# Performance work log

Measured on AMD Instinct MI355X. Metric: run time of the kernel, lower is better.

Reference implementation:

```python
import jax, jax.numpy as jnp
import numpy as np

EMBED = 1024
HEADS = 16
HEAD_DIM = EMBED // HEADS


def setup_inputs() -> dict:
    key = jax.random.key(0)
    ks = jax.random.split(key, 6)
    N, S = 4, 1024
    query = jax.random.normal(ks[0], (N, S, EMBED), dtype=jnp.float32)
    keys = jax.random.normal(ks[1], (N, S, EMBED), dtype=jnp.float32)
    values = jax.random.normal(ks[2], (N, S, EMBED), dtype=jnp.float32)
    mask = jax.random.randint(ks[3], (N, 1, S, S), 0, 2, dtype=jnp.int32)
    W_out = jax.random.normal(ks[4], (EMBED, EMBED), dtype=jnp.float32) * (1.0 / np.sqrt(EMBED))
    b_out = jax.random.normal(ks[5], (EMBED,), dtype=jnp.float32) * 0.02
    return {"query": query, "keys": keys, "values": values, "mask": mask,
            "W_out": W_out, "b_out": b_out}


def reference(query, keys, values, mask, W_out, b_out):
    N, Q, _ = query.shape
    K = keys.shape[1]
    # NOTE: the torch module never applies its per-head q/k/v Linear layers;
    # only the reshape + attention + fc_out are in the forward path.
    q = query.reshape(N, Q, HEADS, HEAD_DIM)
    k = keys.reshape(N, K, HEADS, HEAD_DIM)
    v = values.reshape(N, K, HEADS, HEAD_DIM)
    # energy: [N, H, Q, K]
    energy = jnp.einsum("bqhd,bkhd->bhqk", q, k)
    energy = jnp.where(mask == 0, jnp.float32(-1e20), energy)
    attn = jax.nn.softmax(energy / jnp.sqrt(jnp.float32(HEAD_DIM)), axis=3)
    out = jnp.einsum("bhqk,bkhd->bqhd", attn, v).reshape(N, Q, HEADS * HEAD_DIM)
    return out @ W_out.T + b_out
```

## Files before the change

### kernel.cpp

```cpp
#include <hip/hip_runtime.h>
#include <math.h>

#define NB 4
#define SL 1024
#define EMB 1024
#define NH 16
#define HD 64
#define QB 128

typedef __attribute__((ext_vector_type(8))) short bf16x8;
typedef __attribute__((ext_vector_type(4))) float f32x4;

static __device__ __forceinline__ unsigned pk2(float a, float b) {
    unsigned x = __float_as_uint(a) + 0x8000u;
    unsigned y = __float_as_uint(b) + 0x8000u;
    return (x >> 16) | (y & 0xFFFF0000u);
}
static __device__ __forceinline__ float exp2_fast(float x) {
    float r; asm("v_exp_f32 %0, %1" : "=v"(r) : "v"(x)); return r;
}
static __device__ __forceinline__ void gload_lds16(const void* g, void* l) {
    __builtin_amdgcn_global_load_lds(
        (const __attribute__((address_space(1))) unsigned int*)g,
        (__attribute__((address_space(3))) unsigned int*)l, 16, 0, 0);
}

__global__ __launch_bounds__(256) void prep(
    const float* __restrict__ W, unsigned short* __restrict__ Wb,
    const float* __restrict__ Kf, unsigned short* __restrict__ Kb,
    const float* __restrict__ V, unsigned short* __restrict__ Vt,
    const int* __restrict__ mask, unsigned long long* __restrict__ Mbt)
{
    __shared__ unsigned short sT[128 * 68];
    const int bid = blockIdx.x, tid = threadIdx.x;

    if (bid < 512) {
        int i = (bid * 256 + tid) * 8;
        float4 f0 = *(const float4*)&W[i];
        float4 f1 = *(const float4*)&W[i + 4];
        uint4 u = { pk2(f0.x,f0.y), pk2(f0.z,f0.w), pk2(f1.x,f1.y), pk2(f1.z,f1.w) };
        *(uint4*)&Wb[i] = u;
    } else if (bid < 2560) {
        int t = bid - 512;
        int b = t >> 9, h = (t >> 5) & 15, k0 = (t & 31) * 32;
        int r = tid >> 3, d = (tid & 7) * 8;
        const float* gp = &Kf[((size_t)(b * SL + k0 + r)) * EMB + h * HD + d];
        float4 f0 = *(const float4*)gp, f1 = *(const float4*)(gp + 4);
        uint4 u = { pk2(f0.x,f0.y), pk2(f0.z,f0.w), pk2(f1.x,f1.y), pk2(f1.z,f1.w) };
        *(uint4*)&Kb[((size_t)((b * NH + h) * SL + k0 + r)) * HD + d] = u;
    } else if (bid < 3072) {
        int t = bid - 2560;
        int bh = t >> 3, kb = t & 7;
        int b = bh >> 4, h = bh & 15;
        int k0 = kb * 128;
        #pragma unroll
        for (int i = 0; i < 4; ++i) {
            int lin = (i * 256 + tid) * 8;
            int r = lin >> 6, d = lin & 63;
            const float* gp = &V[((size_t)(b * SL + k0 + r)) * EMB + h * HD + d];
            float4 f0 = *(const float4*)gp, f1 = *(const float4*)(gp + 4);
            uint2 u0 = { pk2(f0.x,f0.y), pk2(f0.z,f0.w) };
            uint2 u1 = { pk2(f1.x,f1.y), pk2(f1.z,f1.w) };
            *(uint2*)&sT[r * 68 + d]     = u0;
            *(uint2*)&sT[r * 68 + d + 4] = u1;
        }
        __syncthreads();
        #pragma unroll
        for (int p = 0; p < 4; ++p) {
            int d = p * 16 + (tid >> 4);
            int c = tid & 15;
            unsigned v[4];
            #pragma unroll
            for (int j = 0; j < 4; ++j) {
                unsigned lo = sT[(c * 8 + 2 * j) * 68 + d];
                unsigned hi = sT[(c * 8 + 2 * j + 1) * 68 + d];
                v[j] = lo | (hi << 16);
            }
            uint4 u = { v[0], v[1], v[2], v[3] };
            *(uint4*)&Vt[((size_t)(bh * HD + d)) * SL + k0 + c * 8] = u;
        }
    } else {
        int t = bid - 3072;
        int lane = tid & 63;
        #pragma unroll
        for (int r = 0; r < 4; ++r) {
            int wid = (t * 4 + (tid >> 6)) * 4 + r;
            int c = wid & 15, q = (wid >> 4) & 1023, bb = wid >> 14;
            int mv = mask[((size_t)bb * SL + q) * SL + c * 64 + lane];
            unsigned long long bits = __ballot(mv != 0);
            if (lane == 0) Mbt[((size_t)bb * 16 + c) * SL + q] = bits;
        }
    }
}

__global__ __launch_bounds__(256, 2) void attn_mfma(
    const float* __restrict__ Q, const unsigned short* __restrict__ Kb,
    const unsigned short* __restrict__ Vt,
    const unsigned long long* __restrict__ Mbt,
    unsigned short* __restrict__ Oa)
{
    const int q0 = blockIdx.x * QB;
    const int h = blockIdx.y, b = blockIdx.z;
    const int tid = threadIdx.x;
    const int w = tid >> 6, lane = tid & 63;
    const int m16 = lane & 15, quad = lane >> 4;
    const int lr = lane >> 3, lc = lane & 7;
    const int sr0 = tid >> 3;

    __shared__ __align__(16) unsigned short sQ[QB * 64];
    __shared__ __align__(16) unsigned short sK[2][64 * 64];
    __shared__ __align__(16) unsigned short sVt[2][64 * 64];
    __shared__ __align__(16) unsigned short sP[QB * 72];
    __shared__ uint2 lut[16];

    if (tid < 16) {
        unsigned w0 = ((tid & 1) ? 0xFFFFu : 0u) | ((tid & 2) ? 0xFFFF0000u : 0u);
        unsigned w1 = ((tid & 4) ? 0xFFFFu : 0u) | ((tid & 8) ? 0xFFFF0000u : 0u);
        lut[tid] = make_uint2(w0, w1);
    }

    const size_t vbase = (size_t)((b * NH + h) * HD) * SL;
    const size_t kbase = (size_t)((b * NH + h) * SL) * HD;

    #pragma unroll
    for (int i = 0; i < 2; ++i) {
        int row = w * 16 + i * 8;
        gload_lds16(&Vt[vbase + (size_t)(row + lr) * SL + (lc ^ lr) * 8], &sVt[0][row * 64]);
        gload_lds16(&Kb[kbase + (size_t)(row + lr) * HD + (lc ^ lr) * 8], &sK[0][row * 64]);
    }
    #pragma unroll
    for (int it = 0; it < 4; ++it) {
        int r = sr0 + it * 32;
        const float* gp = &Q[((size_t)(b * SL + q0 + r)) * EMB + h * HD + lc * 8];
        float4 f0 = *(const float4*)gp, f1 = *(const float4*)(gp + 4);
        uint4 u = { pk2(f0.x,f0.y), pk2(f0.z,f0.w), pk2(f1.x,f1.y), pk2(f1.z,f1.w) };
        *(uint4*)&sQ[r * 64 + ((lc ^ (r & 7)) * 8)] = u;
    }
    __syncthreads();

    bf16x8 bQ[2][2];
    #pragma unroll
    for (int u = 0; u < 2; ++u) {
        int qrow = w * 32 + u * 16 + m16;
        #pragma unroll
        for (int hh = 0; hh < 2; ++hh)
            bQ[u][hh] = *(const bf16x8*)&sQ[qrow * 64 + (((hh * 4 + quad) ^ (qrow & 7)) * 8)];
    }

    f32x4 O[2][4] = {};
    f32x4 lacc[2] = {};
    const float CSC = 0.125f * 1.44269504f;
    const short one_bf = (short)0x3F80;
    const bf16x8 ones = { one_bf, one_bf, one_bf, one_bf, one_bf, one_bf, one_bf, one_bf };

    for (int kt = 0; kt < 16; ++kt) {
        const int bf = kt & 1;
        if (kt < 15) {
            const int k0n = (kt + 1) * 64;
            #pragma unroll
            for (int i = 0; i < 2; ++i) {
                int row = w * 16 + i * 8;
                gload_lds16(&Vt[vbase + (size_t)(row + lr) * SL + k0n + (lc ^ lr) * 8],
                            &sVt[bf ^ 1][row * 64]);
                gload_lds16(&Kb[kbase + (size_t)(k0n + row + lr) * HD + (lc ^ lr) * 8],
                            &sK[bf ^ 1][row * 64]);
            }
        }
        unsigned long long mb0 = Mbt[(size_t)(b * 16 + kt) * SL + q0 + w * 32 + m16];
        unsigned long long mb1 = Mbt[(size_t)(b * 16 + kt) * SL + q0 + w * 32 + 16 + m16];

        f32x4 sc[2][4];
        #pragma unroll
        for (int t = 0; t < 4; ++t) {
            int krow = t * 16 + m16;
            bf16x8 a0 = *(const bf16x8*)&sK[bf][krow * 64 + ((quad ^ (krow & 7)) * 8)];
            bf16x8 a1 = *(const bf16x8*)&sK[bf][krow * 64 + (((4 + quad) ^ (krow & 7)) * 8)];
            f32x4 z = {0.f, 0.f, 0.f, 0.f};
            sc[0][t] = __builtin_amdgcn_mfma_f32_16x16x32_bf16(a0, bQ[0][0], z,        0,0,0);
            sc[0][t] = __builtin_amdgcn_mfma_f32_16x16x32_bf16(a1, bQ[0][1], sc[0][t], 0,0,0);
            sc[1][t] = __builtin_amdgcn_mfma_f32_16x16x32_bf16(a0, bQ[1][0], z,        0,0,0);
            sc[1][t] = __builtin_amdgcn_mfma_f32_16x16x32_bf16(a1, bQ[1][1], sc[1][t], 0,0,0);
        }

        #pragma unroll
        for (int u = 0; u < 2; ++u) {
            unsigned long long mb = u ? mb1 : mb0;
            unsigned wlo = (unsigned)mb, whi = (unsigned)(mb >> 32);
            unsigned short* pr = &sP[(w * 32 + u * 16 + m16) * 72];
            #pragma unroll
            for (int t = 0; t < 4; ++t) {
                unsigned word = (t < 2) ? wlo : whi;
                unsigned nib = (word >> ((t & 1) * 16 + quad * 4)) & 0xFu;
                uint2 am = lut[nib];
                uint2 pw;
                pw.x = pk2(exp2_fast(sc[u][t][0] * CSC), exp2_fast(sc[u][t][1] * CSC)) & am.x;
                pw.y = pk2(exp2_fast(sc[u][t][2] * CSC), exp2_fast(sc[u][t][3] * CSC)) & am.y;
                *(uint2*)&pr[t * 16 + quad * 4] = pw;
            }
        }
        asm volatile("s_waitcnt lgkmcnt(0)" ::: "memory");

        bf16x8 bP[2][2];
        #pragma unroll
        for (int u = 0; u < 2; ++u)
            #pragma unroll
            for (int hh = 0; hh < 2; ++hh)
                bP[u][hh] = *(const bf16x8*)&sP[(w * 32 + u * 16 + m16) * 72 + hh * 32 + quad * 8];

        lacc[0] = __builtin_amdgcn_mfma_f32_16x16x32_bf16(ones, bP[0][0], lacc[0], 0,0,0);
        lacc[0] = __builtin_amdgcn_mfma_f32_16x16x32_bf16(ones, bP[0][1], lacc[0], 0,0,0);
        lacc[1] = __builtin_amdgcn_mfma_f32_16x16x32_bf16(ones, bP[1][0], lacc[1], 0,0,0);
        lacc[1] = __builtin_amdgcn_mfma_f32_16x16x32_bf16(ones, bP[1][1], lacc[1], 0,0,0);

        #pragma unroll
        for (int dt = 0; dt < 4; ++dt) {
            int drow = dt * 16 + m16;
            bf16x8 v0 = *(const bf16x8*)&sVt[bf][drow * 64 + ((quad ^ (drow & 7)) * 8)];
            bf16x8 v1 = *(const bf16x8*)&sVt[bf][drow * 64 + (((4 + quad) ^ (drow & 7)) * 8)];
            O[0][dt] = __builtin_amdgcn_mfma_f32_16x16x32_bf16(v0, bP[0][0], O[0][dt], 0,0,0);
            O[0][dt] = __builtin_amdgcn_mfma_f32_16x16x32_bf16(v1, bP[0][1], O[0][dt], 0,0,0);
            O[1][dt] = __builtin_amdgcn_mfma_f32_16x16x32_bf16(v0, bP[1][0], O[1][dt], 0,0,0);
            O[1][dt] = __builtin_amdgcn_mfma_f32_16x16x32_bf16(v1, bP[1][1], O[1][dt], 0,0,0);
        }

        __syncthreads();
    }

    #pragma unroll
    for (int u = 0; u < 2; ++u) {
        float inv = 1.f / lacc[u][0];
        size_t base = ((size_t)(b * SL + q0 + w * 32 + u * 16 + m16)) * EMB + h * HD + quad * 4;
        #pragma unroll
        for (int dt = 0; dt < 4; ++dt) {
            uint2 ow = { pk2(O[u][dt][0] * inv, O[u][dt][1] * inv),
                         pk2(O[u][dt][2] * inv, O[u][dt][3] * inv) };
            *(uint2*)&Oa[base + dt * 16] = ow;
        }
    }
}

__global__ __launch_bounds__(512, 2) void proj_mfma(
    const unsigned short* __restrict__ A, const unsigned short* __restrict__ Wb,
    const float* __restrict__ bias, float* __restrict__ C)
{
    const int n0 = blockIdx.x * 128;
    const int m0 = blockIdx.y * 128;
    const int tid = threadIdx.x;
    const int w = tid >> 6, lane = tid & 63;
    const int m16 = lane & 15, quad = lane >> 4;
    const int lr = lane >> 3, lc = lane & 7;
    const int wm = (w >> 2) * 64, wn = (w & 3) * 32;

    __shared__ __align__(16) unsigned short sA[2][128 * 64];
    __shared__ __align__(16) unsigned short sW[2][128 * 64];

    f32x4 acc[4][2] = {};

    #pragma unroll
    for (int i = 0; i < 2; ++i) {
        int r = w * 16 + i * 8;
        gload_lds16(&A [(size_t)(m0 + r + lr) * EMB + (lc ^ lr) * 8], &sA[0][r * 64]);
        gload_lds16(&Wb[(size_t)(n0 + r + lr) * EMB + (lc ^ lr) * 8], &sW[0][r * 64]);
    }
    __syncthreads();

    for (int it = 0; it < 16; ++it) {
        const int bf = it & 1;
        if (it < 15) {
            int e0 = (it + 1) * 64;
            #pragma unroll
            for (int i = 0; i < 2; ++i) {
                int r = w * 16 + i * 8;
                gload_lds16(&A [(size_t)(m0 + r + lr) * EMB + e0 + (lc ^ lr) * 8], &sA[bf ^ 1][r * 64]);
                gload_lds16(&Wb[(size_t)(n0 + r + lr) * EMB + e0 + (lc ^ lr) * 8], &sW[bf ^ 1][r * 64]);
            }
        }
        #pragma unroll
        for (int hh = 0; hh < 2; ++hh) {
            bf16x8 af[4], bw[2];
            #pragma unroll
            for (int mt = 0; mt < 4; ++mt) {
                int r = wm + mt * 16 + m16;
                af[mt] = *(const bf16x8*)&sA[bf][r * 64 + (((hh * 4 + quad) ^ (r & 7)) * 8)];
            }
            #pragma unroll
            for (int nt = 0; nt < 2; ++nt) {
                int r = wn + nt * 16 + m16;
                bw[nt] = *(const bf16x8*)&sW[bf][r * 64 + (((hh * 4 + quad) ^ (r & 7)) * 8)];
            }
            #pragma unroll
            for (int mt = 0; mt < 4; ++mt)
                #pragma unroll
                for (int nt = 0; nt < 2; ++nt)
                    acc[mt][nt] = __builtin_amdgcn_mfma_f32_16x16x32_bf16(af[mt], bw[nt], acc[mt][nt], 0,0,0);
        }
        __syncthreads();
    }

    #pragma unroll
    for (int nt = 0; nt < 2; ++nt) {
        float bv = bias[n0 + wn + nt * 16 + m16];
        #pragma unroll
        for (int mt = 0; mt < 4; ++mt) {
            size_t row = (size_t)(m0 + wm + mt * 16 + quad * 4);
            #pragma unroll
            for (int rg = 0; rg < 4; ++rg)
                C[(row + rg) * EMB + n0 + wn + nt * 16 + m16] = acc[mt][nt][rg] + bv;
        }
    }
}

extern "C" void kernel_launch(void* const* d_in, const int* in_sizes, int n_in,
                              void* d_out, int out_size, void* d_ws, size_t ws_size,
                              hipStream_t stream) {
    const float* Q    = (const float*)d_in[0];
    const float* K    = (const float*)d_in[1];
    const float* V    = (const float*)d_in[2];
    const int*   mask = (const int*)  d_in[3];
    const float* W    = (const float*)d_in[4];
    const float* bias = (const float*)d_in[5];

    unsigned short* Oa = (unsigned short*)d_ws;
    unsigned short* Wb = Oa + (size_t)NB * SL * EMB;
    unsigned long long* Mbt = (unsigned long long*)(Wb + (size_t)EMB * EMB);
    unsigned short* Vt = (unsigned short*)(Mbt + (size_t)NB * 16 * SL);
    unsigned short* Kb = Vt + (size_t)NB * NH * HD * SL;

    prep<<<7168, 256, 0, stream>>>(W, Wb, K, Kb, V, Vt, mask, Mbt);
    attn_mfma<<<dim3(SL / QB, NH, NB), 256, 0, stream>>>(Q, Kb, Vt, Mbt, Oa);
    proj_mfma<<<dim3(EMB / 128, (NB * SL) / 128), 512, 0, stream>>>(Oa, Wb, bias, (float*)d_out);
}
```

Before: 165.8 us.

## Triple-buffer K/V loads with vmcnt waits, XCD-aware block mapping, and merged Q/P LDS

Replaces the double-buffered K/V pipeline with a three-stage ring that prefetches two tiles ahead. Each tile waits on explicit s_waitcnt vmcnt counts and a single raw barrier, replacing the trailing __syncthreads. Mask words are prefetched two iterations ahead in registers, and Q staging shares LDS with the P buffer. The grid is linearised with an XCD-aware mapping so blocks of the same batch-head land on the same XCD for L2 reuse of K/V, and s_setprio brackets the MFMA sections. The hand-counted vmcnt values and buffer aliasing are fragile and could cause races if the counts are wrong.

```diff
diff --git a/kernel.cpp b/kernel.cpp
--- a/kernel.cpp
+++ b/kernel.cpp
@@ -24,6 +24,9 @@
         (const __attribute__((address_space(1))) unsigned int*)g,
         (__attribute__((address_space(3))) unsigned int*)l, 16, 0, 0);
 }
+
+#define VMW(n) asm volatile("s_waitcnt vmcnt(" #n ")" ::: "memory")
+#define MEMPIN() asm volatile("" ::: "memory")
 
 __global__ __launch_bounds__(256) void prep(
     const float* __restrict__ W, unsigned short* __restrict__ Wb,
@@ -99,18 +102,20 @@
     const unsigned long long* __restrict__ Mbt,
     unsigned short* __restrict__ Oa)
 {
-    const int q0 = blockIdx.x * QB;
-    const int h = blockIdx.y, b = blockIdx.z;
+    const int lin = blockIdx.x;
+    const int xcd = lin & 7, slot = lin >> 3;
+    const int bh = xcd * 8 + (slot >> 3);
+    const int q0 = (slot & 7) * QB;
+    const int b = bh >> 4, h = bh & 15;
     const int tid = threadIdx.x;
     const int w = tid >> 6, lane = tid & 63;
     const int m16 = lane & 15, quad = lane >> 4;
     const int lr = lane >> 3, lc = lane & 7;
     const int sr0 = tid >> 3;
 
-    __shared__ __align__(16) unsigned short sQ[QB * 64];
-    __shared__ __align__(16) unsigned short sK[2][64 * 64];
-    __shared__ __align__(16) unsigned short sVt[2][64 * 64];
-    __shared__ __align__(16) unsigned short sP[QB * 72];
+    __shared__ __align__(16) unsigned short sK[3][64 * 64];
+    __shared__ __align__(16) unsigned short sVt[3][64 * 64];
+    __shared__ __align__(16) unsigned short sPQ[QB * 72];
     __shared__ uint2 lut[16];
 
     if (tid < 16) {
@@ -119,24 +124,50 @@
         lut[tid] = make_uint2(w0, w1);
     }
 
-    const size_t vbase = (size_t)((b * NH + h) * HD) * SL;
-    const size_t kbase = (size_t)((b * NH + h) * SL) * HD;
-
+    const size_t vbase = (size_t)(bh * HD) * SL;
+    const size_t kbase = (size_t)(bh * SL) * HD;
+    const size_t mbase = (size_t)(b * 16) * SL + q0 + w * 32 + m16;
+
+    float4 qf[4][2];
+    #pragma unroll
+    for (int it = 0; it < 4; ++it) {
+        int r = sr0 + it * 32;
+        const float* gp = &Q[((size_t)(b * SL + q0 + r)) * EMB + h * HD + lc * 8];
+        qf[it][0] = *(const float4*)gp;
+        qf[it][1] = *(const float4*)(gp + 4);
+    }
+    MEMPIN();
+    unsigned long long mbA0, mbA1, mbB0, mbB1, mbC0 = 0, mbC1 = 0;
     #pragma unroll
     for (int i = 0; i < 2; ++i) {
         int row = w * 16 + i * 8;
         gload_lds16(&Vt[vbase + (size_t)(row + lr) * SL + (lc ^ lr) * 8], &sVt[0][row * 64]);
         gload_lds16(&Kb[kbase + (size_t)(row + lr) * HD + (lc ^ lr) * 8], &sK[0][row * 64]);
     }
+    MEMPIN();
+    mbA0 = Mbt[mbase];
+    mbA1 = Mbt[mbase + 16];
+    MEMPIN();
+    #pragma unroll
+    for (int i = 0; i < 2; ++i) {
+        int row = w * 16 + i * 8;
+        gload_lds16(&Vt[vbase + (size_t)(row + lr) * SL + 64 + (lc ^ lr) * 8], &sVt[1][row * 64]);
+        gload_lds16(&Kb[kbase + (size_t)(64 + row + lr) * HD + (lc ^ lr) * 8], &sK[1][row * 64]);
+    }
+    MEMPIN();
+    mbB0 = Mbt[mbase + SL];
+    mbB1 = Mbt[mbase + SL + 16];
+    MEMPIN();
     #pragma unroll
     for (int it = 0; it < 4; ++it) {
         int r = sr0 + it * 32;
-        const float* gp = &Q[((size_t)(b * SL + q0 + r)) * EMB + h * HD + lc * 8];
-        float4 f0 = *(const float4*)gp, f1 = *(const float4*)(gp + 4);
-        uint4 u = { pk2(f0.x,f0.y), pk2(f0.z,f0.w), pk2(f1.x,f1.y), pk2(f1.z,f1.w) };
-        *(uint4*)&sQ[r * 64 + ((lc ^ (r & 7)) * 8)] = u;
-    }
-    __syncthreads();
+        uint4 u = { pk2(qf[it][0].x, qf[it][0].y), pk2(qf[it][0].z, qf[it][0].w),
+                    pk2(qf[it][1].x, qf[it][1].y), pk2(qf[it][1].z, qf[it][1].w) };
+        *(uint4*)&sPQ[r * 72 + ((lc ^ (r & 7)) * 8)] = u;
+    }
+    asm volatile("s_waitcnt lgkmcnt(0)" ::: "memory");
+    __builtin_amdgcn_s_barrier();
+    __builtin_amdgcn_sched_barrier(0);
 
     bf16x8 bQ[2][2];
     #pragma unroll
@@ -144,8 +175,15 @@
         int qrow = w * 32 + u * 16 + m16;
         #pragma unroll
         for (int hh = 0; hh < 2; ++hh)
-            bQ[u][hh] = *(const bf16x8*)&sQ[qrow * 64 + (((hh * 4 + quad) ^ (qrow & 7)) * 8)];
-    }
+            bQ[u][hh] = *(const bf16x8*)&sPQ[qrow * 72 + (((hh * 4 + quad) ^ (qrow & 7)) * 8)];
+    }
+
+    unsigned short* kc = (unsigned short*)sK[0];
+    unsigned short* kn = (unsigned short*)sK[1];
+    unsigned short* k2 = (unsigned short*)sK[2];
+    unsigned short* vc = (unsigned short*)sVt[0];
+    unsigned short* vn = (unsigned short*)sVt[1];
+    unsigned short* v2 = (unsigned short*)sVt[2];
 
     f32x4 O[2][4] = {};
     f32x4 lacc[2] = {};
@@ -154,39 +192,46 @@
     const bf16x8 ones = { one_bf, one_bf, one_bf, one_bf, one_bf, one_bf, one_bf, one_bf };
 
     for (int kt = 0; kt < 16; ++kt) {
-        const int bf = kt & 1;
-        if (kt < 15) {
-            const int k0n = (kt + 1) * 64;
+        if (kt < 15) { VMW(8); } else { VMW(2); }
+        __builtin_amdgcn_s_barrier();
+        __builtin_amdgcn_sched_barrier(0);
+
+        if (kt < 14) {
+            const int k0n = (kt + 2) * 64;
             #pragma unroll
             for (int i = 0; i < 2; ++i) {
                 int row = w * 16 + i * 8;
                 gload_lds16(&Vt[vbase + (size_t)(row + lr) * SL + k0n + (lc ^ lr) * 8],
-                            &sVt[bf ^ 1][row * 64]);
+                            &v2[row * 64]);
                 gload_lds16(&Kb[kbase + (size_t)(k0n + row + lr) * HD + (lc ^ lr) * 8],
-                            &sK[bf ^ 1][row * 64]);
-            }
-        }
-        unsigned long long mb0 = Mbt[(size_t)(b * 16 + kt) * SL + q0 + w * 32 + m16];
-        unsigned long long mb1 = Mbt[(size_t)(b * 16 + kt) * SL + q0 + w * 32 + 16 + m16];
+                            &k2[row * 64]);
+            }
+            MEMPIN();
+            mbC0 = Mbt[mbase + (size_t)(kt + 2) * SL];
+            mbC1 = Mbt[mbase + (size_t)(kt + 2) * SL + 16];
+            MEMPIN();
+        }
 
         f32x4 sc[2][4];
+        __builtin_amdgcn_s_setprio(1);
         #pragma unroll
         for (int t = 0; t < 4; ++t) {
             int krow = t * 16 + m16;
-            bf16x8 a0 = *(const bf16x8*)&sK[bf][krow * 64 + ((quad ^ (krow & 7)) * 8)];
-            bf16x8 a1 = *(const bf16x8*)&sK[bf][krow * 64 + (((4 + quad) ^ (krow & 7)) * 8)];
+            bf16x8 a0 = *(const bf16x8*)&kc[krow * 64 + ((quad ^ (krow & 7)) * 8)];
+            bf16x8 a1 = *(const bf16x8*)&kc[krow * 64 + (((4 + quad) ^ (krow & 7)) * 8)];
             f32x4 z = {0.f, 0.f, 0.f, 0.f};
             sc[0][t] = __builtin_amdgcn_mfma_f32_16x16x32_bf16(a0, bQ[0][0], z,        0,0,0);
             sc[0][t] = __builtin_amdgcn_mfma_f32_16x16x32_bf16(a1, bQ[0][1], sc[0][t], 0,0,0);
             sc[1][t] = __builtin_amdgcn_mfma_f32_16x16x32_bf16(a0, bQ[1][0], z,        0,0,0);
             sc[1][t] = __builtin_amdgcn_mfma_f32_16x16x32_bf16(a1, bQ[1][1], sc[1][t], 0,0,0);
         }
+        __builtin_amdgcn_s_setprio(0);
 
         #pragma unroll
         for (int u = 0; u < 2; ++u) {
-            unsigned long long mb = u ? mb1 : mb0;
+            unsigned long long mb = u ? mbA1 : mbA0;
             unsigned wlo = (unsigned)mb, whi = (unsigned)(mb >> 32);
-            unsigned short* pr = &sP[(w * 32 + u * 16 + m16) * 72];
+            unsigned short* pr = &sPQ[(w * 32 + u * 16 + m16) * 72];
             #pragma unroll
             for (int t = 0; t < 4; ++t) {
                 unsigned word = (t < 2) ? wlo : whi;
@@ -205,8 +250,9 @@
         for (int u = 0; u < 2; ++u)
             #pragma unroll
             for (int hh = 0; hh < 2; ++hh)
-                bP[u][hh] = *(const bf16x8*)&sP[(w * 32 + u * 16 + m16) * 72 + hh * 32 + quad * 8];
-
+                bP[u][hh] = *(const bf16x8*)&sPQ[(w * 32 + u * 16 + m16) * 72 + hh * 32 + quad * 8];
+
+        __builtin_amdgcn_s_setprio(1);
         lacc[0] = __builtin_amdgcn_mfma_f32_16x16x32_bf16(ones, bP[0][0], lacc[0], 0,0,0);
         lacc[0] = __builtin_amdgcn_mfma_f32_16x16x32_bf16(ones, bP[0][1], lacc[0], 0,0,0);
         lacc[1] = __builtin_amdgcn_mfma_f32_16x16x32_bf16(ones, bP[1][0], lacc[1], 0,0,0);
@@ -215,15 +261,18 @@
         #pragma unroll
         for (int dt = 0; dt < 4; ++dt) {
             int drow = dt * 16 + m16;
-            bf16x8 v0 = *(const bf16x8*)&sVt[bf][drow * 64 + ((quad ^ (drow & 7)) * 8)];
-            bf16x8 v1 = *(const bf16x8*)&sVt[bf][drow * 64 + (((4 + quad) ^ (drow & 7)) * 8)];
+            bf16x8 v0 = *(const bf16x8*)&vc[drow * 64 + ((quad ^ (drow & 7)) * 8)];
+            bf16x8 v1 = *(const bf16x8*)&vc[drow * 64 + (((4 + quad) ^ (drow & 7)) * 8)];
             O[0][dt] = __builtin_amdgcn_mfma_f32_16x16x32_bf16(v0, bP[0][0], O[0][dt], 0,0,0);
             O[0][dt] = __builtin_amdgcn_mfma_f32_16x16x32_bf16(v1, bP[0][1], O[0][dt], 0,0,0);
             O[1][dt] = __builtin_amdgcn_mfma_f32_16x16x32_bf16(v0, bP[1][0], O[1][dt], 0,0,0);
             O[1][dt] = __builtin_amdgcn_mfma_f32_16x16x32_bf16(v1, bP[1][1], O[1][dt], 0,0,0);
         }
-
-        __syncthreads();
+        __builtin_amdgcn_s_setprio(0);
+
+        unsigned short* tk = kc; kc = kn; kn = k2; k2 = tk;
+        unsigned short* tv = vc; vc = vn; vn = v2; v2 = tv;
+        mbA0 = mbB0; mbA1 = mbB1; mbB0 = mbC0; mbB1 = mbC1;
     }
 
     #pragma unroll
@@ -327,6 +376,6 @@
     unsigned short* Kb = Vt + (size_t)NB * NH * HD * SL;
 
     prep<<<7168, 256, 0, stream>>>(W, Wb, K, Kb, V, Vt, mask, Mbt);
-    attn_mfma<<<dim3(SL / QB, NH, NB), 256, 0, stream>>>(Q, Kb, Vt, Mbt, Oa);
+    attn_mfma<<<512, 256, 0, stream>>>(Q, Kb, Vt, Mbt, Oa);
     proj_mfma<<<dim3(EMB / 128, (NB * SL) / 128), 512, 0, stream>>>(Oa, Wb, bias, (float*)d_out);
 }
```

New measurement: 162.6 us. No clear change (-1.9%).
